# Performance work log

Measured on AMD Instinct MI355X. Metric: run time of the kernel, lower is better.

The kernel has to match this reference:

```python
import jax, jax.numpy as jnp
import numpy as np

N_NODES = 100000
N_EDGES = 1600000
F_IN = 128
HID = 128
LAT = 64
NUM_LAYERS = 3
NUM_GRAPHS = 512


def setup_inputs() -> dict:
    key = jax.random.key(0)
    ks = jax.random.split(key, 12)
    x = jax.random.normal(ks[0], (N_NODES, F_IN), dtype=jnp.float32)
    edge_index = jax.random.randint(ks[1], (2, N_EDGES), 0, N_NODES, dtype=jnp.int64)
    batch = jnp.sort(jax.random.randint(ks[2], (N_NODES,), 0, NUM_GRAPHS, dtype=jnp.int32))
    s_in = 1.0 / np.sqrt(F_IN)
    s_h = 1.0 / np.sqrt(HID)
    W_in = jax.random.uniform(ks[3], (F_IN, HID), jnp.float32, -s_in, s_in)
    b_in = jax.random.uniform(ks[4], (HID,), jnp.float32, -s_in, s_in)
    W_msg = jax.random.uniform(ks[5], (NUM_LAYERS, HID, HID), jnp.float32, -s_h, s_h)
    b_msg = jax.random.uniform(ks[6], (NUM_LAYERS, HID), jnp.float32, -s_h, s_h)
    W_upd = jax.random.uniform(ks[7], (NUM_LAYERS, HID, HID), jnp.float32, -s_h, s_h)
    b_upd = jax.random.uniform(ks[8], (NUM_LAYERS, HID), jnp.float32, -s_h, s_h)
    W_mean = jax.random.uniform(ks[9], (HID, LAT), jnp.float32, -s_h, s_h)
    b_mean = jax.random.uniform(ks[10], (LAT,), jnp.float32, -s_h, s_h)
    W_logvar = jax.random.uniform(ks[11], (HID, LAT), jnp.float32, -s_h, s_h)
    b_logvar = jax.random.uniform(jax.random.fold_in(key, 99), (LAT,), jnp.float32, -s_h, s_h)
    return {"x": x, "edge_index": edge_index, "batch": batch,
            "W_in": W_in, "b_in": b_in, "W_msg": W_msg, "b_msg": b_msg,
            "W_upd": W_upd, "b_upd": b_upd, "W_mean": W_mean, "b_mean": b_mean,
            "W_logvar": W_logvar, "b_logvar": b_logvar}


def _mp_layer(h, src, dst, Wm, bm, Wu, bu):
    # message: Linear+ReLU on all nodes, gather per-edge, scatter-add into dst
    messages = jax.nn.relu(h @ Wm + bm)                      # [N, H]
    agg = jax.ops.segment_sum(messages[src], dst, num_segments=N_NODES)  # [N, H]
    return jax.nn.relu(agg @ Wu + bu) + h                    # update + residual


def reference(x, edge_index, batch, W_in, b_in, W_msg, b_msg, W_upd, b_upd,
              W_mean, b_mean, W_logvar, b_logvar):
    src = edge_index[0]
    dst = edge_index[1]
    h = jax.nn.relu(x @ W_in + b_in)
    for l in range(NUM_LAYERS):
        h = _mp_layer(h, src, dst, W_msg[l], b_msg[l], W_upd[l], b_upd[l])
    # graph-level sum pooling by batch segment ids
    g = jax.ops.segment_sum(h, batch, num_segments=NUM_GRAPHS)  # [G, H]
    z_mean = g @ W_mean + b_mean
    z_logvar = g @ W_logvar + b_logvar
    return (z_mean, z_logvar)
```

## Files before the change

kernel.cpp:

```cpp
#include <hip/hip_runtime.h>
#include <hip/hip_bf16.h>
#include <cstdint>

#define N_NODES 100000
#define N_EDGES 1600000
#define N_GRAPHS 512
#define N_LAYERS 3
#define NB 1563
#define BCAP 2048
#define NFB 256

typedef __bf16 bf16x8 __attribute__((ext_vector_type(8)));
typedef float f32x4 __attribute__((ext_vector_type(4)));
typedef uint uint4v __attribute__((ext_vector_type(4)));

__device__ __forceinline__ float bf2f(ushort u) {
  uint v = ((uint)u) << 16;
  return __builtin_bit_cast(float, v);
}
__device__ __forceinline__ ushort f2bf(float f) {
  uint u = __builtin_bit_cast(uint, f);
  u += 0x7FFF + ((u >> 16) & 1);
  return (ushort)(u >> 16);
}
__device__ __forceinline__ uint pk2(float lo, float hi) {
  return (uint)f2bf(lo) | ((uint)f2bf(hi) << 16);
}

__global__ void k_detect64(const int* __restrict__ e, int* __restrict__ flag) {
  if (threadIdx.x == 0 && blockIdx.x == 0) {
    int any = 0;
    for (int i = 1; i < 128; i += 2) any |= e[i];
    *flag = (any == 0) ? 1 : 0;
  }
}

__global__ __launch_bounds__(256) void k_cvt_edges(const int* __restrict__ e32,
    const long long* __restrict__ e64, const int* __restrict__ flag,
    int* __restrict__ es, int* __restrict__ ds) {
  int i = blockIdx.x * 256 + threadIdx.x;
  if (i >= N_EDGES) return;
  if (*flag) { es[i] = (int)e64[i]; ds[i] = (int)e64[N_EDGES + i]; }
  else       { es[i] = e32[i];      ds[i] = e32[N_EDGES + i]; }
}

__global__ __launch_bounds__(256) void k_bfill3(const int* __restrict__ es,
    const int* __restrict__ ds, int* __restrict__ bcur, uint* __restrict__ packed) {
  __shared__ int lcnt[NB];
  __shared__ int lbase[NB];
  const int t = threadIdx.x;
  const int e0 = blockIdx.x * (N_EDGES / NFB);
  const int e1 = e0 + (N_EDGES / NFB);
  for (int k = t; k < NB; k += 256) lcnt[k] = 0;
  __syncthreads();
  for (int i = e0 + t; i < e1; i += 256)
    atomicAdd(&lcnt[ds[i] >> 6], 1);
  __syncthreads();
  for (int k = t; k < NB; k += 256) {
    int c = lcnt[k];
    lbase[k] = (c > 0) ? atomicAdd(&bcur[k * 16], c) : 0;
    lcnt[k] = 0;
  }
  __syncthreads();
  for (int i = e0 + t; i < e1; i += 256) {
    int d = ds[i], s = es[i];
    int bk = d >> 6;
    int pos = lbase[bk] + atomicAdd(&lcnt[bk], 1);
    if (pos < BCAP)
      packed[(size_t)bk * BCAP + pos] = ((uint)(d & 63) << 17) | (uint)s;
  }
}

__global__ __launch_bounds__(256) void k_bsort(const int* __restrict__ bcur,
    const uint* __restrict__ packed, uint* __restrict__ srcs,
    int* __restrict__ nbeg, int* __restrict__ nend) {
  __shared__ uint sp[BCAP];
  __shared__ uint so[BCAP];
  __shared__ int cnt[64], pref[64], cur[64];
  const int bk = blockIdx.x, t = threadIdx.x;
  const int c = min(bcur[bk * 16], BCAP);
  if (t < 64) cnt[t] = 0;
  __syncthreads();
  for (int i = t; i < c; i += 256) {
    uint p = packed[(size_t)bk * BCAP + i];
    sp[i] = p;
    atomicAdd(&cnt[p >> 17], 1);
  }
  __syncthreads();
  if (t == 0) {
    int run = 0;
    #pragma unroll
    for (int j = 0; j < 64; ++j) { pref[j] = run; run += cnt[j]; }
  }
  if (t < 64) cur[t] = 0;
  __syncthreads();
  for (int i = t; i < c; i += 256) {
    uint p = sp[i];
    int n = p >> 17;
    int pos = atomicAdd(&cur[n], 1);
    so[pref[n] + pos] = min(p & 0x1FFFF, (uint)(N_NODES - 1));
  }
  __syncthreads();
  for (int i = t; i < c; i += 256) srcs[(size_t)bk * BCAP + i] = so[i];
  if (t < 64) {
    int base = bk * BCAP;
    nbeg[bk * 64 + t] = base + pref[t];
    nend[bk * 64 + t] = base + pref[t] + cnt[t];
  }
}

__global__ __launch_bounds__(256) void k_prep_w(const float* __restrict__ W_in,
    const float* __restrict__ W_msg, const float* __restrict__ W_upd,
    ushort* __restrict__ Wt) {
  int b = blockIdx.x;
  const float* W = (b == 0) ? W_in : (b <= 3 ? W_msg + (size_t)(b - 1) * 16384
                                             : W_upd + (size_t)(b - 4) * 16384);
  ushort* O = Wt + (size_t)b * 16384;
  for (int i = threadIdx.x; i < 16384; i += 256) {
    int k = i >> 7, c = i & 127;
    O[c * 128 + k] = f2bf(W[i]);
  }
}

template <bool CVT, bool RES>
__global__ __launch_bounds__(256) void k_gemm_bf16(const ushort* __restrict__ Ab,
    const float* __restrict__ Af, const ushort* __restrict__ Wt,
    const float* __restrict__ bias, const ushort* __restrict__ res,
    ushort* __restrict__ out) {
  __shared__ ushort sA[64][136];
  const int t = threadIdx.x;
  const int row0 = blockIdx.x * 64;
  const int lane = t & 63;
  const int col0 = (t >> 6) * 32;
  const int lr = lane & 15, lk = (lane >> 4) * 8;

  bf16x8 bfr[4][2];
  #pragma unroll
  for (int kk = 0; kk < 4; ++kk) {
    bfr[kk][0] = *(const bf16x8*)&Wt[(col0 + lr) * 128 + kk * 32 + lk];
    bfr[kk][1] = *(const bf16x8*)&Wt[(col0 + 16 + lr) * 128 + kk * 32 + lk];
  }

  #pragma unroll
  for (int i = 0; i < 4; ++i) {
    int c = t + 256 * i;
    int r = c >> 4, k8 = (c & 15) * 8;
    int gr = min(row0 + r, N_NODES - 1);
    if (CVT) {
      const float* src = &Af[(size_t)gr * 128 + k8];
      float4 x0 = *(const float4*)src;
      float4 x1 = *(const float4*)(src + 4);
      uint4v u;
      u.x = pk2(x0.x, x0.y); u.y = pk2(x0.z, x0.w);
      u.z = pk2(x1.x, x1.y); u.w = pk2(x1.z, x1.w);
      *(uint4v*)&sA[r][k8] = u;
    } else {
      *(uint4*)&sA[r][k8] = *(const uint4*)&Ab[(size_t)gr * 128 + k8];
    }
  }
  __syncthreads();

  f32x4 acc[4][2] = {};
  #pragma unroll
  for (int kk = 0; kk < 4; ++kk) {
    int kb = kk * 32 + lk;
    #pragma unroll
    for (int m = 0; m < 4; ++m) {
      bf16x8 a = *(const bf16x8*)&sA[m * 16 + lr][kb];
      acc[m][0] = __builtin_amdgcn_mfma_f32_16x16x32_bf16(a, bfr[kk][0], acc[m][0], 0, 0, 0);
      acc[m][1] = __builtin_amdgcn_mfma_f32_16x16x32_bf16(a, bfr[kk][1], acc[m][1], 0, 0, 0);
    }
  }

  const int rb = (lane >> 4) * 4;
  #pragma unroll
  for (int n = 0; n < 2; ++n) {
    int col = col0 + n * 16 + lr;
    float bv = bias[col];
    #pragma unroll
    for (int m = 0; m < 4; ++m) {
      #pragma unroll
      for (int j = 0; j < 4; ++j) {
        int r = row0 + m * 16 + rb + j;
        if (r < N_NODES) {
          float v = fmaxf(acc[m][n][j] + bv, 0.f);
          if (RES) v += bf2f(res[(size_t)r * 128 + col]);
          out[(size_t)r * 128 + col] = f2bf(v);
        }
      }
    }
  }
}

__global__ __launch_bounds__(256) void k_aggregate(const int* __restrict__ nbeg,
    const int* __restrict__ nend, const uint* __restrict__ srcs,
    const ushort* __restrict__ msg, ushort* __restrict__ agg) {
  int wid = blockIdx.x * 4 + (threadIdx.x >> 6);
  if (wid >= N_NODES) return;
  const int lane = threadIdx.x & 63;
  const int sub = lane >> 4, l16 = lane & 15;
  int e = nbeg[wid];
  const int en = nend[wid];
  float a[8] = {0.f, 0.f, 0.f, 0.f, 0.f, 0.f, 0.f, 0.f};

  for (; e + 8 <= en; e += 8) {
    uint s0 = srcs[e + sub];
    uint s1 = srcs[e + 4 + sub];
    uint4 m0 = *(const uint4*)&msg[(size_t)s0 * 128 + l16 * 8];
    uint4 m1 = *(const uint4*)&msg[(size_t)s1 * 128 + l16 * 8];
    a[0] += bf2f((ushort)m0.x) + bf2f((ushort)m1.x);
    a[1] += bf2f((ushort)(m0.x >> 16)) + bf2f((ushort)(m1.x >> 16));
    a[2] += bf2f((ushort)m0.y) + bf2f((ushort)m1.y);
    a[3] += bf2f((ushort)(m0.y >> 16)) + bf2f((ushort)(m1.y >> 16));
    a[4] += bf2f((ushort)m0.z) + bf2f((ushort)m1.z);
    a[5] += bf2f((ushort)(m0.z >> 16)) + bf2f((ushort)(m1.z >> 16));
    a[6] += bf2f((ushort)m0.w) + bf2f((ushort)m1.w);
    a[7] += bf2f((ushort)(m0.w >> 16)) + bf2f((ushort)(m1.w >> 16));
  }
  if (e + 4 <= en) {
    uint s0 = srcs[e + sub];
    uint4 m0 = *(const uint4*)&msg[(size_t)s0 * 128 + l16 * 8];
    a[0] += bf2f((ushort)m0.x);
    a[1] += bf2f((ushort)(m0.x >> 16));
    a[2] += bf2f((ushort)m0.y);
    a[3] += bf2f((ushort)(m0.y >> 16));
    a[4] += bf2f((ushort)m0.z);
    a[5] += bf2f((ushort)(m0.z >> 16));
    a[6] += bf2f((ushort)m0.w);
    a[7] += bf2f((ushort)(m0.w >> 16));
    e += 4;
  }
  int rem = en - e;
  if (sub < rem) {
    uint s0 = srcs[e + sub];
    uint4 m0 = *(const uint4*)&msg[(size_t)s0 * 128 + l16 * 8];
    a[0] += bf2f((ushort)m0.x);
    a[1] += bf2f((ushort)(m0.x >> 16));
    a[2] += bf2f((ushort)m0.y);
    a[3] += bf2f((ushort)(m0.y >> 16));
    a[4] += bf2f((ushort)m0.z);
    a[5] += bf2f((ushort)(m0.z >> 16));
    a[6] += bf2f((ushort)m0.w);
    a[7] += bf2f((ushort)(m0.w >> 16));
  }

  #pragma unroll
  for (int j = 0; j < 8; ++j) {
    a[j] += __shfl_xor(a[j], 16, 64);
    a[j] += __shfl_xor(a[j], 32, 64);
  }
  if (sub == 0) {
    uint4 r;
    r.x = pk2(a[0], a[1]);
    r.y = pk2(a[2], a[3]);
    r.z = pk2(a[4], a[5]);
    r.w = pk2(a[6], a[7]);
    *(uint4*)&agg[(size_t)wid * 128 + l16 * 8] = r;
  }
}

__global__ __launch_bounds__(128) void k_pool(const ushort* __restrict__ h,
    const int* __restrict__ batch, float* __restrict__ g) {
  int t = threadIdx.x;
  int v0 = blockIdx.x * 128;
  int v1 = min(v0 + 128, N_NODES);
  if (v0 >= N_NODES) return;
  int cur = batch[v0];
  float acc = 0.f;
  for (int v = v0; v < v1; ++v) {
    int b = batch[v];
    if (b != cur) {
      unsafeAtomicAdd(&g[cur * 128 + t], acc);
      acc = 0.f;
      cur = b;
    }
    acc += bf2f(h[(size_t)v * 128 + t]);
  }
  unsafeAtomicAdd(&g[cur * 128 + t], acc);
}

__global__ __launch_bounds__(128) void k_head(const float* __restrict__ g,
    const float* __restrict__ Wm, const float* __restrict__ bm,
    const float* __restrict__ Wl, const float* __restrict__ bl,
    float* __restrict__ out) {
  __shared__ float sg[128];
  int gr = blockIdx.x, t = threadIdx.x;
  sg[t] = g[gr * 128 + t];
  __syncthreads();
  const float* W = (t < 64) ? Wm : Wl;
  const float* b = (t < 64) ? bm : bl;
  int c = t & 63;
  float acc = b[c];
  #pragma unroll 8
  for (int k = 0; k < 128; ++k) acc += sg[k] * W[k * 64 + c];
  out[(size_t)(t < 64 ? 0 : N_GRAPHS * 64) + (size_t)gr * 64 + c] = acc;
}

extern "C" void kernel_launch(void* const* d_in, const int* in_sizes, int n_in,
                              void* d_out, int out_size, void* d_ws, size_t ws_size,
                              hipStream_t stream) {
  const float* x      = (const float*)d_in[0];
  const int* e32      = (const int*)d_in[1];
  const long long* e64 = (const long long*)d_in[1];
  const int* batch    = (const int*)d_in[2];
  const float* W_in   = (const float*)d_in[3];
  const float* b_in   = (const float*)d_in[4];
  const float* W_msg  = (const float*)d_in[5];
  const float* b_msg  = (const float*)d_in[6];
  const float* W_upd  = (const float*)d_in[7];
  const float* b_upd  = (const float*)d_in[8];
  const float* W_mean = (const float*)d_in[9];
  const float* b_mean = (const float*)d_in[10];
  const float* W_lv   = (const float*)d_in[11];
  const float* b_lv   = (const float*)d_in[12];
  float* out = (float*)d_out;

  char* p = (char*)d_ws;
  auto alloc = [&](size_t bytes) {
    char* r = p;
    p += (bytes + 255) & ~(size_t)255;
    return r;
  };
  ushort* bufA   = (ushort*)alloc((size_t)N_NODES * 128 * 2);
  ushort* bufB   = (ushort*)alloc((size_t)N_NODES * 128 * 2);
  ushort* bufM   = (ushort*)alloc((size_t)N_NODES * 128 * 2);
  ushort* Wt     = (ushort*)alloc((size_t)7 * 16384 * 2);
  uint*   packed = (uint*)alloc((size_t)NB * BCAP * 4);
  uint*   srcs   = (uint*)alloc((size_t)NB * BCAP * 4);
  int*    es     = (int*)alloc((size_t)N_EDGES * 4);
  int*    dsb    = (int*)alloc((size_t)N_EDGES * 4);
  int*    bcur   = (int*)alloc((size_t)NB * 16 * 4);
  int*    nbeg   = (int*)alloc((size_t)NB * 64 * 4);
  int*    nend   = (int*)alloc((size_t)NB * 64 * 4);
  int*    flag   = (int*)alloc(64 * 4);
  float*  g      = (float*)alloc((size_t)N_GRAPHS * 128 * 4);

  hipMemsetAsync(bcur, 0, (size_t)NB * 16 * 4, stream);
  hipMemsetAsync(g, 0, (size_t)N_GRAPHS * 128 * 4, stream);

  k_detect64<<<1, 64, 0, stream>>>(e32, flag);
  k_cvt_edges<<<(N_EDGES + 255) / 256, 256, 0, stream>>>(e32, e64, flag, es, dsb);
  k_bfill3<<<NFB, 256, 0, stream>>>(es, dsb, bcur, packed);
  k_bsort<<<NB, 256, 0, stream>>>(bcur, packed, srcs, nbeg, nend);

  k_prep_w<<<7, 256, 0, stream>>>(W_in, W_msg, W_upd, Wt);

  const int GB = NB;

  k_gemm_bf16<true, false><<<GB, 256, 0, stream>>>(nullptr, x, Wt, b_in, nullptr, bufA);

  ushort* h = bufA;
  ushort* hn = bufB;
  for (int l = 0; l < N_LAYERS; ++l) {
    const ushort* Wm = Wt + (size_t)(1 + l) * 16384;
    const float* bm = b_msg + (size_t)l * 128;
    const ushort* Wu = Wt + (size_t)(4 + l) * 16384;
    const float* bu = b_upd + (size_t)l * 128;
    k_gemm_bf16<false, false><<<GB, 256, 0, stream>>>(h, nullptr, Wm, bm, nullptr, bufM);
    k_aggregate<<<(N_NODES + 3) / 4, 256, 0, stream>>>(nbeg, nend, srcs, bufM, hn);
    k_gemm_bf16<false, true><<<GB, 256, 0, stream>>>(hn, nullptr, Wu, bu, h, hn);
    ushort* sw = h; h = hn; hn = sw;
  }

  k_pool<<<(N_NODES + 127) / 128, 128, 0, stream>>>(h, batch, g);
  k_head<<<N_GRAPHS, 128, 0, stream>>>(g, W_mean, b_mean, W_lv, b_lv, out);
}
```

Before: 465.1 us.

## Fuse update GEMM with next layer's message GEMM, unroll aggregation gather

Each update GEMM now writes its output tile back into shared memory and immediately runs the next layer's message GEMM on it, so the separate message-GEMM launch and its reread of h are gone. The input projection is fused with the first message GEMM in the same way. The aggregation loop now issues four gathers per iteration with a unified tail and 32-bit index math. Pooling uses 256-thread blocks. This adds a third buffer, more registers per block and an extra barrier in the fused GEMM.

```diff
diff --git a/kernel.cpp b/kernel.cpp
--- a/kernel.cpp
+++ b/kernel.cpp
@@ -122,11 +122,13 @@
   }
 }
 
-template <bool CVT, bool RES>
-__global__ __launch_bounds__(256) void k_gemm_bf16(const ushort* __restrict__ Ab,
-    const float* __restrict__ Af, const ushort* __restrict__ Wt,
-    const float* __restrict__ bias, const ushort* __restrict__ res,
-    ushort* __restrict__ out) {
+template <bool CVT, bool RES, bool SECOND>
+__global__ __launch_bounds__(256) void k_gemm2(const ushort* __restrict__ Ab,
+    const float* __restrict__ Af,
+    const ushort* __restrict__ W1, const float* __restrict__ b1,
+    const ushort* __restrict__ res, ushort* __restrict__ out1,
+    const ushort* __restrict__ W2, const float* __restrict__ b2,
+    ushort* __restrict__ out2) {
   __shared__ ushort sA[64][136];
   const int t = threadIdx.x;
   const int row0 = blockIdx.x * 64;
@@ -137,8 +139,8 @@
   bf16x8 bfr[4][2];
   #pragma unroll
   for (int kk = 0; kk < 4; ++kk) {
-    bfr[kk][0] = *(const bf16x8*)&Wt[(col0 + lr) * 128 + kk * 32 + lk];
-    bfr[kk][1] = *(const bf16x8*)&Wt[(col0 + 16 + lr) * 128 + kk * 32 + lk];
+    bfr[kk][0] = *(const bf16x8*)&W1[(col0 + lr) * 128 + kk * 32 + lk];
+    bfr[kk][1] = *(const bf16x8*)&W1[(col0 + 16 + lr) * 128 + kk * 32 + lk];
   }
 
   #pragma unroll
@@ -172,20 +174,59 @@
     }
   }
 
+  bf16x8 bfr2[4][2];
+  if (SECOND) {
+    #pragma unroll
+    for (int kk = 0; kk < 4; ++kk) {
+      bfr2[kk][0] = *(const bf16x8*)&W2[(col0 + lr) * 128 + kk * 32 + lk];
+      bfr2[kk][1] = *(const bf16x8*)&W2[(col0 + 16 + lr) * 128 + kk * 32 + lk];
+    }
+    __syncthreads();
+  }
+
   const int rb = (lane >> 4) * 4;
   #pragma unroll
   for (int n = 0; n < 2; ++n) {
     int col = col0 + n * 16 + lr;
-    float bv = bias[col];
+    float bv = b1[col];
     #pragma unroll
     for (int m = 0; m < 4; ++m) {
       #pragma unroll
       for (int j = 0; j < 4; ++j) {
         int r = row0 + m * 16 + rb + j;
-        if (r < N_NODES) {
-          float v = fmaxf(acc[m][n][j] + bv, 0.f);
-          if (RES) v += bf2f(res[(size_t)r * 128 + col]);
-          out[(size_t)r * 128 + col] = f2bf(v);
+        float v = fmaxf(acc[m][n][j] + bv, 0.f);
+        if (RES && r < N_NODES) v += bf2f(res[(size_t)r * 128 + col]);
+        ushort hv = f2bf(v);
+        if (r < N_NODES) out1[(size_t)r * 128 + col] = hv;
+        if (SECOND) sA[m * 16 + rb + j][col] = hv;
+      }
+    }
+  }
+
+  if (SECOND) {
+    __syncthreads();
+    f32x4 acc2[4][2] = {};
+    #pragma unroll
+    for (int kk = 0; kk < 4; ++kk) {
+      int kb = kk * 32 + lk;
+      #pragma unroll
+      for (int m = 0; m < 4; ++m) {
+        bf16x8 a = *(const bf16x8*)&sA[m * 16 + lr][kb];
+        acc2[m][0] = __builtin_amdgcn_mfma_f32_16x16x32_bf16(a, bfr2[kk][0], acc2[m][0], 0, 0, 0);
+        acc2[m][1] = __builtin_amdgcn_mfma_f32_16x16x32_bf16(a, bfr2[kk][1], acc2[m][1], 0, 0, 0);
+      }
+    }
+    #pragma unroll
+    for (int n = 0; n < 2; ++n) {
+      int col = col0 + n * 16 + lr;
+      float bv = b2[col];
+      #pragma unroll
+      for (int m = 0; m < 4; ++m) {
+        #pragma unroll
+        for (int j = 0; j < 4; ++j) {
+          int r = row0 + m * 16 + rb + j;
+          if (r < N_NODES)
+            out2[(size_t)r * 128 + col] = f2bf(fmaxf(acc2[m][n][j] + bv, 0.f));
         }
       }
     }
@@ -198,51 +239,39 @@
   int wid = blockIdx.x * 4 + (threadIdx.x >> 6);
   if (wid >= N_NODES) return;
   const int lane = threadIdx.x & 63;
-  const int sub = lane >> 4, l16 = lane & 15;
+  const uint sub = lane >> 4, l16 = lane & 15;
   int e = nbeg[wid];
   const int en = nend[wid];
   float a[8] = {0.f, 0.f, 0.f, 0.f, 0.f, 0.f, 0.f, 0.f};
 
-  for (; e + 8 <= en; e += 8) {
+#define ACC8(mv)                                              \
+  a[0] += bf2f((ushort)mv.x); a[1] += bf2f((ushort)(mv.x >> 16)); \
+  a[2] += bf2f((ushort)mv.y); a[3] += bf2f((ushort)(mv.y >> 16)); \
+  a[4] += bf2f((ushort)mv.z); a[5] += bf2f((ushort)(mv.z >> 16)); \
+  a[6] += bf2f((ushort)mv.w); a[7] += bf2f((ushort)(mv.w >> 16));
+
+  for (; e + 16 <= en; e += 16) {
     uint s0 = srcs[e + sub];
     uint s1 = srcs[e + 4 + sub];
-    uint4 m0 = *(const uint4*)&msg[(size_t)s0 * 128 + l16 * 8];
-    uint4 m1 = *(const uint4*)&msg[(size_t)s1 * 128 + l16 * 8];
-    a[0] += bf2f((ushort)m0.x) + bf2f((ushort)m1.x);
-    a[1] += bf2f((ushort)(m0.x >> 16)) + bf2f((ushort)(m1.x >> 16));
-    a[2] += bf2f((ushort)m0.y) + bf2f((ushort)m1.y);
-    a[3] += bf2f((ushort)(m0.y >> 16)) + bf2f((ushort)(m1.y >> 16));
-    a[4] += bf2f((ushort)m0.z) + bf2f((ushort)m1.z);
-    a[5] += bf2f((ushort)(m0.z >> 16)) + bf2f((ushort)(m1.z >> 16));
-    a[6] += bf2f((ushort)m0.w) + bf2f((ushort)m1.w);
-    a[7] += bf2f((ushort)(m0.w >> 16)) + bf2f((ushort)(m1.w >> 16));
-  }
-  if (e + 4 <= en) {
-    uint s0 = srcs[e + sub];
-    uint4 m0 = *(const uint4*)&msg[(size_t)s0 * 128 + l16 * 8];
-    a[0] += bf2f((ushort)m0.x);
-    a[1] += bf2f((ushort)(m0.x >> 16));
-    a[2] += bf2f((ushort)m0.y);
-    a[3] += bf2f((ushort)(m0.y >> 16));
-    a[4] += bf2f((ushort)m0.z);
-    a[5] += bf2f((ushort)(m0.z >> 16));
-    a[6] += bf2f((ushort)m0.w);
-    a[7] += bf2f((ushort)(m0.w >> 16));
-    e += 4;
-  }
-  int rem = en - e;
-  if (sub < rem) {
-    uint s0 = srcs[e + sub];
-    uint4 m0 = *(const uint4*)&msg[(size_t)s0 * 128 + l16 * 8];
-    a[0] += bf2f((ushort)m0.x);
-    a[1] += bf2f((ushort)(m0.x >> 16));
-    a[2] += bf2f((ushort)m0.y);
-    a[3] += bf2f((ushort)(m0.y >> 16));
-    a[4] += bf2f((ushort)m0.z);
-    a[5] += bf2f((ushort)(m0.z >> 16));
-    a[6] += bf2f((ushort)m0.w);
-    a[7] += bf2f((ushort)(m0.w >> 16));
-  }
+    uint s2 = srcs[e + 8 + sub];
+    uint s3 = srcs[e + 12 + sub];
+    uint4 m0 = *(const uint4*)&msg[s0 * 128u + l16 * 8u];
+    uint4 m1 = *(const uint4*)&msg[s1 * 128u + l16 * 8u];
+    uint4 m2 = *(const uint4*)&msg[s2 * 128u + l16 * 8u];
+    uint4 m3 = *(const uint4*)&msg[s3 * 128u + l16 * 8u];
+    ACC8(m0) ACC8(m1) ACC8(m2) ACC8(m3)
+  }
+  const uint rem = (uint)(en - e);
+  #pragma unroll
+  for (uint k = 0; k < 4; ++k) {
+    uint idx = k * 4 + sub;
+    if (idx < rem) {
+      uint s = srcs[e + idx];
+      uint4 m = *(const uint4*)&msg[s * 128u + l16 * 8u];
+      ACC8(m)
+    }
+  }
+#undef ACC8
 
   #pragma unroll
   for (int j = 0; j < 8; ++j) {
@@ -259,10 +288,11 @@
   }
 }
 
-__global__ __launch_bounds__(128) void k_pool(const ushort* __restrict__ h,
+__global__ __launch_bounds__(256) void k_pool(const ushort* __restrict__ h,
     const int* __restrict__ batch, float* __restrict__ g) {
-  int t = threadIdx.x;
-  int v0 = blockIdx.x * 128;
+  int t = threadIdx.x & 127;
+  int half = threadIdx.x >> 7;
+  int v0 = blockIdx.x * 256 + half * 128;
   int v1 = min(v0 + 128, N_NODES);
   if (v0 >= N_NODES) return;
   int cur = batch[v0];
@@ -323,6 +353,7 @@
   };
   ushort* bufA   = (ushort*)alloc((size_t)N_NODES * 128 * 2);
   ushort* bufB   = (ushort*)alloc((size_t)N_NODES * 128 * 2);
+  ushort* bufC   = (ushort*)alloc((size_t)N_NODES * 128 * 2);
   ushort* bufM   = (ushort*)alloc((size_t)N_NODES * 128 * 2);
   ushort* Wt     = (ushort*)alloc((size_t)7 * 16384 * 2);
   uint*   packed = (uint*)alloc((size_t)NB * BCAP * 4);
@@ -346,22 +377,28 @@
   k_prep_w<<<7, 256, 0, stream>>>(W_in, W_msg, W_upd, Wt);
 
   const int GB = NB;
-
-  k_gemm_bf16<true, false><<<GB, 256, 0, stream>>>(nullptr, x, Wt, b_in, nullptr, bufA);
+  const ushort* Wm[3] = {Wt + 16384, Wt + 2 * 16384, Wt + 3 * 16384};
+  const ushort* Wu[3] = {Wt + 4 * 16384, Wt + 5 * 16384, Wt + 6 * 16384};
+
+  k_gemm2<true, false, true><<<GB, 256, 0, stream>>>(
+      nullptr, x, Wt, b_in, nullptr, bufA, Wm[0], b_msg, bufM);
 
   ushort* h = bufA;
   ushort* hn = bufB;
   for (int l = 0; l < N_LAYERS; ++l) {
-    const ushort* Wm = Wt + (size_t)(1 + l) * 16384;
-    const float* bm = b_msg + (size_t)l * 128;
-    const ushort* Wu = Wt + (size_t)(4 + l) * 16384;
-    const float* bu = b_upd + (size_t)l * 128;
-    k_gemm_bf16<false, false><<<GB, 256, 0, stream>>>(h, nullptr, Wm, bm, nullptr, bufM);
-    k_aggregate<<<(N_NODES + 3) / 4, 256, 0, stream>>>(nbeg, nend, srcs, bufM, hn);
-    k_gemm_bf16<false, true><<<GB, 256, 0, stream>>>(hn, nullptr, Wu, bu, h, hn);
+    k_aggregate<<<(N_NODES + 3) / 4, 256, 0, stream>>>(nbeg, nend, srcs, bufM, bufC);
+    if (l < N_LAYERS - 1) {
+      k_gemm2<false, true, true><<<GB, 256, 0, stream>>>(
+          bufC, nullptr, Wu[l], b_upd + (size_t)l * 128, h, hn,
+          Wm[l + 1], b_msg + (size_t)(l + 1) * 128, bufM);
+    } else {
+      k_gemm2<false, true, false><<<GB, 256, 0, stream>>>(
+          bufC, nullptr, Wu[l], b_upd + (size_t)l * 128, h, hn,
+          nullptr, nullptr, nullptr);
+    }
     ushort* sw = h; h = hn; hn = sw;
   }
 
-  k_pool<<<(N_NODES + 127) / 128, 128, 0, stream>>>(h, batch, g);
+  k_pool<<<(N_NODES + 255) / 256, 256, 0, stream>>>(h, batch, g);
   k_head<<<N_GRAPHS, 128, 0, stream>>>(g, W_mean, b_mean, W_lv, b_lv, out);
 }
```

Result: slower. 487.8 us, median of 5 (+4.9%).
